# Kernel tuning notes

Hardware: AMD Instinct MI355X
Metric: run time of the kernel (lower is better)

Reference implementation:

```python
import jax, jax.numpy as jnp
import numpy as np

N_NODES = 65536
N_EDGES = 524288
N_GRAPHS = 64
PTS_PER_GRAPH = 1024


def gcn_conv(x, W, b, row, col, self_idx, n_nodes):
    # PyG GCNConv: x' = D^{-1/2} (A + I) D^{-1/2} x W + b
    xw = x @ W
    row2 = jnp.concatenate([row, self_idx])
    col2 = jnp.concatenate([col, self_idx])
    deg = jax.ops.segment_sum(jnp.ones_like(col2, dtype=xw.dtype), col2, num_segments=n_nodes)
    dinv = jax.lax.rsqrt(deg)  # deg >= 1 thanks to self-loops
    norm = dinv[row2] * dinv[col2]  # [E+N]
    out = jax.ops.segment_sum(xw[row2] * norm[:, None], col2, num_segments=n_nodes)
    return out + b


def setup_inputs() -> dict:
    key = jax.random.key(0)
    ks = jax.random.split(key, 12)

    def glorot(k, fan_in, fan_out):
        s = jnp.sqrt(6.0 / (fan_in + fan_out))
        return jax.random.uniform(k, (fan_in, fan_out), jnp.float32, -s, s)

    x = jax.random.normal(ks[0], (N_NODES, 3), jnp.float32)
    edge_index = jax.random.randint(ks[1], (2, N_EDGES), 0, N_NODES, dtype=jnp.int64)
    batch = (jnp.arange(N_NODES, dtype=jnp.int64) // PTS_PER_GRAPH)  # 64 graphs x 1024 pts

    return {
        "x": x, "edge_index": edge_index, "batch": batch,
        "W1": glorot(ks[2], 3, 64), "b1": jnp.zeros((64,), jnp.float32),
        "W2": glorot(ks[3], 64, 256), "b2": jnp.zeros((256,), jnp.float32),
        "W3": glorot(ks[4], 256, 512), "b3": jnp.zeros((512,), jnp.float32),
        "Wm1": glorot(ks[5], 1024, 512), "bm1": jnp.zeros((512,), jnp.float32),
        "Wm2": glorot(ks[6], 512, 10), "bm2": jnp.zeros((10,), jnp.float32),
    }


def reference(x, edge_index, batch, W1, b1, W2, b2, W3, b3, Wm1, bm1, Wm2, bm2):
    n = x.shape[0]
    row, col = edge_index[0], edge_index[1]
    self_idx = jnp.arange(n, dtype=edge_index.dtype)

    x1 = jax.nn.relu(gcn_conv(x, W1, b1, row, col, self_idx, n))
    x2 = jax.nn.relu(gcn_conv(x1, W2, b2, row, col, self_idx, n))
    x3 = jax.nn.relu(gcn_conv(x2, W3, b3, row, col, self_idx, n))

    # global mean / max pool over batch segments
    counts = jax.ops.segment_sum(jnp.ones((n,), x3.dtype), batch, num_segments=N_GRAPHS)
    x_mean = jax.ops.segment_sum(x3, batch, num_segments=N_GRAPHS) / counts[:, None]
    x_max = jax.ops.segment_max(x3, batch, num_segments=N_GRAPHS)
    h = jnp.concatenate([x_mean, x_max], axis=1)  # [G, 1024]

    h = jax.nn.relu(h @ Wm1 + bm1)  # dropout is identity in eval
    return h @ Wm2 + bm2  # [G, 10]
```

## Files before the change

kernel.cpp:

```cpp
#include <hip/hip_runtime.h>
#include <hip/hip_bf16.h>

typedef __hip_bfloat16 bf16;
typedef short bf16x8 __attribute__((ext_vector_type(8)));
typedef float f32x4 __attribute__((ext_vector_type(4)));

__device__ __forceinline__ float b2f_us(unsigned short u) {
    union { unsigned int i; float f; } c;
    c.i = ((unsigned int)u) << 16;
    return c.f;
}
__device__ __forceinline__ unsigned short f2b_us(float f) {
    bf16 h = __float2bfloat16(f);
    return *reinterpret_cast<unsigned short*>(&h);
}
__device__ __forceinline__ void unpack8(uint4 p, float* f) {
    f[0] = b2f_us(p.x & 0xffff); f[1] = b2f_us(p.x >> 16);
    f[2] = b2f_us(p.y & 0xffff); f[3] = b2f_us(p.y >> 16);
    f[4] = b2f_us(p.z & 0xffff); f[5] = b2f_us(p.z >> 16);
    f[6] = b2f_us(p.w & 0xffff); f[7] = b2f_us(p.w >> 16);
}

__device__ __forceinline__ void async_copy16(const bf16* g, bf16* l) {
    __builtin_amdgcn_global_load_lds(
        (const __attribute__((address_space(1))) unsigned int*)g,
        (__attribute__((address_space(3))) unsigned int*)l, 16, 0, 0);
}

__global__ __launch_bounds__(256) void k_count(const int* __restrict__ col,
                                               int* __restrict__ cnt, int E) {
    int e = blockIdx.x * 256 + threadIdx.x;
    if (e < E) atomicAdd(cnt + col[e], 1);
}
__global__ __launch_bounds__(256) void k_scan_a(const int* __restrict__ cnt,
                                                int* __restrict__ bsum,
                                                float* __restrict__ dinv) {
    __shared__ int s[256];
    int t = threadIdx.x;
    int i = blockIdx.x * 256 + t;
    int c = cnt[i];
    dinv[i] = rsqrtf((float)c + 1.0f);
    s[t] = c;
    __syncthreads();
#pragma unroll
    for (int off = 128; off >= 1; off >>= 1) {
        if (t < off) s[t] += s[t + off];
        __syncthreads();
    }
    if (t == 0) bsum[blockIdx.x] = s[0];
}
__global__ __launch_bounds__(256) void k_scan_b(const int* __restrict__ bsum,
                                                int* __restrict__ boff) {
    __shared__ int s[256];
    int t = threadIdx.x;
    int self = bsum[t];
    s[t] = self;
    __syncthreads();
#pragma unroll
    for (int off = 1; off < 256; off <<= 1) {
        int v = (t >= off) ? s[t - off] : 0;
        __syncthreads();
        s[t] += v;
        __syncthreads();
    }
    boff[t] = s[t] - self;
}
__global__ __launch_bounds__(256) void k_scan_c(const int* __restrict__ cnt,
                                                const int* __restrict__ boff,
                                                int* __restrict__ rowptr) {
    __shared__ int s[256];
    int t = threadIdx.x;
    int base = blockIdx.x * 256;
    int self = cnt[base + t];
    s[t] = self;
    __syncthreads();
#pragma unroll
    for (int off = 1; off < 256; off <<= 1) {
        int v = (t >= off) ? s[t - off] : 0;
        __syncthreads();
        s[t] += v;
        __syncthreads();
    }
    rowptr[base + t] = boff[blockIdx.x] + s[t] - self;
}

__global__ __launch_bounds__(256) void k_scatter(const int* __restrict__ row,
                                                 const int* __restrict__ col,
                                                 const float* __restrict__ dinv,
                                                 const int* __restrict__ rowptr,
                                                 int* __restrict__ fill,
                                                 int2* __restrict__ adj, int E) {
    int e = blockIdx.x * 256 + threadIdx.x;
    if (e >= E) return;
    int r = row[e], c = col[e];
    int pos = rowptr[c] + atomicAdd(fill + c, 1);
    adj[pos] = make_int2(r, __float_as_int(dinv[r]));
}

__global__ __launch_bounds__(256) void k_prep_all(const float* __restrict__ W2,
                                                  bf16* __restrict__ WT2,
                                                  const float* __restrict__ W3,
                                                  bf16* __restrict__ WT3) {
    int idx = blockIdx.x * 256 + threadIdx.x;
    if (idx < 64 * 256) {
        int k = idx >> 8, n = idx & 255;
        WT2[n * 64 + k] = __float2bfloat16(W2[idx]);
    } else {
        int i = idx - 64 * 256;
        if (i < 256 * 512) {
            int k = i >> 9, n = i & 511;
            WT3[(size_t)n * 256 + k] = __float2bfloat16(W3[i]);
        }
    }
}

__global__ __launch_bounds__(256) void k_gcn1(const int2* __restrict__ adj,
                                              const int* __restrict__ rowptr,
                                              const int* __restrict__ cnt,
                                              const float* __restrict__ dinv,
                                              const float* __restrict__ x,
                                              const float* __restrict__ W,
                                              const float* __restrict__ bias,
                                              bf16* __restrict__ h1, int N) {
    __shared__ float w[256];
    int t = threadIdx.x;
    if (t < 192) w[t] = W[t];
    else w[t] = bias[t - 192];
    __syncthreads();
    int n = blockIdx.x * 256 + t;
    if (n >= N) return;
    float d = dinv[n];
    float d2 = d * d;
    float a0 = x[n * 3] * d2, a1 = x[n * 3 + 1] * d2, a2 = x[n * 3 + 2] * d2;
    int beg = rowptr[n], end = beg + cnt[n];
    for (int e = beg; e < end; ++e) {
        int2 ad = adj[e];
        float wt = __int_as_float(ad.y) * d;
        a0 += x[ad.x * 3] * wt;
        a1 += x[ad.x * 3 + 1] * wt;
        a2 += x[ad.x * 3 + 2] * wt;
    }
    bf16* dst = h1 + (size_t)n * 64;
#pragma unroll
    for (int fb = 0; fb < 8; ++fb) {
        uint4 r;
        unsigned v[4];
#pragma unroll
        for (int p = 0; p < 4; ++p) {
            int f0 = fb * 8 + p * 2;
            float u0 = fmaxf(a0 * w[f0] + a1 * w[64 + f0] + a2 * w[128 + f0] + w[192 + f0], 0.f);
            int f1 = f0 + 1;
            float u1 = fmaxf(a0 * w[f1] + a1 * w[64 + f1] + a2 * w[128 + f1] + w[192 + f1], 0.f);
            v[p] = (unsigned)f2b_us(u0) | ((unsigned)f2b_us(u1) << 16);
        }
        r.x = v[0]; r.y = v[1]; r.z = v[2]; r.w = v[3];
        *reinterpret_cast<uint4*>(dst + fb * 8) = r;
    }
}

template <int F>
__global__ __launch_bounds__(256, 4) void k_gather_pre(const int2* __restrict__ adj,
                                                       const int* __restrict__ rowptr,
                                                       const int* __restrict__ cnt,
                                                       const float* __restrict__ dinv,
                                                       const bf16* __restrict__ h,
                                                       bf16* __restrict__ agg, int N) {
    constexpr int LPN = F / 8;
    constexpr int NPB = 256 / LPN;
    int t = threadIdx.x;
    int node = blockIdx.x * NPB + t / LPN;
    if (node >= N) return;
    int fbase = (t % LPN) * 8;
    float d = dinv[node];
    size_t sbase = (size_t)node * F + fbase;
    uint4 sp = *reinterpret_cast<const uint4*>(h + sbase);
    float a[8];
    unpack8(sp, a);
    float d2 = d * d;
#pragma unroll
    for (int i = 0; i < 8; i++) a[i] *= d2;
    int beg = rowptr[node];
    int end = beg + cnt[node];
    int e = beg;
    for (; e + 7 < end; e += 8) {
        int2 ad[8];
        uint4 p[8];
#pragma unroll
        for (int u = 0; u < 8; ++u) ad[u] = adj[e + u];
#pragma unroll
        for (int u = 0; u < 8; ++u)
            p[u] = *reinterpret_cast<const uint4*>(h + (size_t)ad[u].x * F + fbase);
#pragma unroll
        for (int u = 0; u < 8; ++u) {
            float wt = __int_as_float(ad[u].y) * d;
            float f[8];
            unpack8(p[u], f);
#pragma unroll
            for (int i = 0; i < 8; i++) a[i] += f[i] * wt;
        }
    }
    for (; e + 3 < end; e += 4) {
        int2 ad[4];
        uint4 p[4];
#pragma unroll
        for (int u = 0; u < 4; ++u) ad[u] = adj[e + u];
#pragma unroll
        for (int u = 0; u < 4; ++u)
            p[u] = *reinterpret_cast<const uint4*>(h + (size_t)ad[u].x * F + fbase);
#pragma unroll
        for (int u = 0; u < 4; ++u) {
            float wt = __int_as_float(ad[u].y) * d;
            float f[8];
            unpack8(p[u], f);
#pragma unroll
            for (int i = 0; i < 8; i++) a[i] += f[i] * wt;
        }
    }
    for (; e < end; ++e) {
        int2 ad = adj[e];
        float wt = __int_as_float(ad.y) * d;
        uint4 p = *reinterpret_cast<const uint4*>(h + (size_t)ad.x * F + fbase);
        float f[8];
        unpack8(p, f);
#pragma unroll
        for (int i = 0; i < 8; i++) a[i] += f[i] * wt;
    }
    uint4 r;
    r.x = (unsigned)f2b_us(a[0]) | ((unsigned)f2b_us(a[1]) << 16);
    r.y = (unsigned)f2b_us(a[2]) | ((unsigned)f2b_us(a[3]) << 16);
    r.z = (unsigned)f2b_us(a[4]) | ((unsigned)f2b_us(a[5]) << 16);
    r.w = (unsigned)f2b_us(a[6]) | ((unsigned)f2b_us(a[7]) << 16);
    *reinterpret_cast<uint4*>(agg + sbase) = r;
}

__global__ __launch_bounds__(256) void k_gemm_br(const bf16* __restrict__ A,
                                                 const bf16* __restrict__ BT,
                                                 const float* __restrict__ bias,
                                                 bf16* __restrict__ C,
                                                 int M, int N, int K) {
    __shared__ bf16 As[128 * 32];
    __shared__ bf16 Bs[128 * 32];
    const int t = threadIdx.x;
    const int wave = t >> 6, lane = t & 63;
    const int quad = lane >> 4, l16 = lane & 15;
    const int wm = wave & 1, wn = wave >> 1;
    const int m0 = blockIdx.x * 128;
    const int n0 = blockIdx.y * 128;

    f32x4 acc[4][4] = {};
    for (int kb = 0; kb < K; kb += 32) {
#pragma unroll
        for (int rnd = 0; rnd < 2; ++rnd) {
            int c = (rnd * 4 + wave) * 64 + lane;
            int r = c >> 2, seg = c & 3;
            async_copy16(A + (size_t)(m0 + r) * K + kb + seg * 8, As + c * 8);
            async_copy16(BT + (size_t)(n0 + r) * K + kb + seg * 8, Bs + c * 8);
        }
        __syncthreads();
        bf16x8 af[4], bfr[4];
#pragma unroll
        for (int i = 0; i < 4; i++)
            af[i] = *reinterpret_cast<const bf16x8*>(&As[(wm * 64 + i * 16 + l16) * 32 + quad * 8]);
#pragma unroll
        for (int j = 0; j < 4; j++)
            bfr[j] = *reinterpret_cast<const bf16x8*>(&Bs[(wn * 64 + j * 16 + l16) * 32 + quad * 8]);
#pragma unroll
        for (int i = 0; i < 4; i++)
#pragma unroll
            for (int j = 0; j < 4; j++)
                acc[i][j] = __builtin_amdgcn_mfma_f32_16x16x32_bf16(af[i], bfr[j], acc[i][j], 0, 0, 0);
        __syncthreads();
    }
#pragma unroll
    for (int j = 0; j < 4; j++) {
        int cn = n0 + wn * 64 + j * 16 + l16;
        float bv = bias[cn];
#pragma unroll
        for (int i = 0; i < 4; i++) {
            int row = m0 + wm * 64 + i * 16 + quad * 4;
#pragma unroll
            for (int r = 0; r < 4; r++)
                C[(size_t)(row + r) * N + cn] = __float2bfloat16(fmaxf(acc[i][j][r] + bv, 0.f));
        }
    }
}

__global__ __launch_bounds__(256) void k_gemm_pool(const bf16* __restrict__ A,
                                                   const bf16* __restrict__ BT,
                                                   const float* __restrict__ bias,
                                                   float* __restrict__ partials,
                                                   int M, int N, int K) {
    __shared__ bf16 As[128 * 32];
    __shared__ bf16 Bs[128 * 32];
    const int t = threadIdx.x;
    const int wave = t >> 6, lane = t & 63;
    const int quad = lane >> 4, l16 = lane & 15;
    const int wm = wave & 1, wn = wave >> 1;
    const int m0 = blockIdx.x * 128;
    const int n0 = blockIdx.y * 128;

    f32x4 acc[4][4] = {};
    for (int kb = 0; kb < K; kb += 32) {
#pragma unroll
        for (int rnd = 0; rnd < 2; ++rnd) {
            int c = (rnd * 4 + wave) * 64 + lane;
            int r = c >> 2, seg = c & 3;
            async_copy16(A + (size_t)(m0 + r) * K + kb + seg * 8, As + c * 8);
            async_copy16(BT + (size_t)(n0 + r) * K + kb + seg * 8, Bs + c * 8);
        }
        __syncthreads();
        bf16x8 af[4], bfr[4];
#pragma unroll
        for (int i = 0; i < 4; i++)
            af[i] = *reinterpret_cast<const bf16x8*>(&As[(wm * 64 + i * 16 + l16) * 32 + quad * 8]);
#pragma unroll
        for (int j = 0; j < 4; j++)
            bfr[j] = *reinterpret_cast<const bf16x8*>(&Bs[(wn * 64 + j * 16 + l16) * 32 + quad * 8]);
#pragma unroll
        for (int i = 0; i < 4; i++)
#pragma unroll
            for (int j = 0; j < 4; j++)
                acc[i][j] = __builtin_amdgcn_mfma_f32_16x16x32_bf16(af[i], bfr[j], acc[i][j], 0, 0, 0);
        __syncthreads();
    }
    size_t pbase = ((size_t)(blockIdx.x * 4 + blockIdx.y) * 2 + wm) * 256;
#pragma unroll
    for (int j = 0; j < 4; j++) {
        int f128 = wn * 64 + j * 16 + l16;
        float bv = bias[n0 + f128];
        float s = 0.f, mx = 0.f;
#pragma unroll
        for (int i = 0; i < 4; i++)
#pragma unroll
            for (int r = 0; r < 4; r++) {
                float v = fmaxf(acc[i][j][r] + bv, 0.f);
                s += v;
                mx = fmaxf(mx, v);
            }
        s += __shfl_xor(s, 16);
        s += __shfl_xor(s, 32);
        mx = fmaxf(mx, __shfl_xor(mx, 16));
        mx = fmaxf(mx, __shfl_xor(mx, 32));
        if (quad == 0) {
            partials[pbase + f128] = s;
            partials[pbase + 128 + f128] = mx;
        }
    }
}

__global__ __launch_bounds__(256) void k_pool_final(const float* __restrict__ partials,
                                                    float* __restrict__ pooled) {
    int idx = blockIdx.x * 256 + threadIdx.x;
    int g = idx >> 9, f = idx & 511;
    int by = f >> 7, f128 = f & 127;
    float S = 0.f, M = 0.f;
#pragma unroll
    for (int tile = 0; tile < 8; ++tile) {
        int bx = g * 8 + tile;
#pragma unroll
        for (int wm = 0; wm < 2; ++wm) {
            size_t pbase = ((size_t)(bx * 4 + by) * 2 + wm) * 256;
            S += partials[pbase + f128];
            M = fmaxf(M, partials[pbase + 128 + f128]);
        }
    }
    pooled[g * 1024 + f] = S * (1.0f / 1024.0f);
    pooled[g * 1024 + 512 + f] = M;
}

__global__ __launch_bounds__(256) void k_mlp1(const float* __restrict__ pooled,
                                              const float* __restrict__ Wm1,
                                              const float* __restrict__ bm1,
                                              float* __restrict__ o) {
    __shared__ float hg[1024];
    __shared__ float red[256];
    int g = blockIdx.x;
    int t = threadIdx.x;
    int f64 = t & 63, kq = t >> 6;
    int f = blockIdx.y * 64 + f64;
#pragma unroll
    for (int i = 0; i < 4; i++) hg[t + i * 256] = pooled[g * 1024 + t + i * 256];
    __syncthreads();
    float acc = 0.f;
    int k0 = kq * 256;
#pragma unroll 8
    for (int k = k0; k < k0 + 256; ++k)
        acc += hg[k] * Wm1[(size_t)k * 512 + f];
    red[t] = acc;
    __syncthreads();
    if (t < 64) {
        float total = red[t] + red[t + 64] + red[t + 128] + red[t + 192] + bm1[f];
        o[g * 512 + f] = fmaxf(total, 0.f);
    }
}

__global__ __launch_bounds__(512) void k_mlp2(const float* __restrict__ h,
                                              const float* __restrict__ Wm2,
                                              const float* __restrict__ bm2,
                                              float* __restrict__ out) {
    int g = blockIdx.x;
    int t = threadIdx.x;
    int j = t >> 5, lane32 = t & 31;
    float acc = 0.f;
    if (j < 10) {
        int k0 = lane32 * 16;
#pragma unroll
        for (int i = 0; i < 16; ++i)
            acc += h[g * 512 + k0 + i] * Wm2[(size_t)(k0 + i) * 10 + j];
    }
#pragma unroll
    for (int m = 16; m >= 1; m >>= 1) acc += __shfl_xor(acc, m);
    if (j < 10 && lane32 == 0) out[g * 10 + j] = acc + bm2[j];
}

extern "C" void kernel_launch(void* const* d_in, const int* in_sizes, int n_in,
                              void* d_out, int out_size, void* d_ws, size_t ws_size,
                              hipStream_t stream) {
    const float* x   = (const float*)d_in[0];
    const int*   ei  = (const int*)d_in[1];
    const float* W1  = (const float*)d_in[3];
    const float* b1  = (const float*)d_in[4];
    const float* W2  = (const float*)d_in[5];
    const float* b2  = (const float*)d_in[6];
    const float* W3  = (const float*)d_in[7];
    const float* b3  = (const float*)d_in[8];
    const float* Wm1 = (const float*)d_in[9];
    const float* bm1 = (const float*)d_in[10];
    const float* Wm2 = (const float*)d_in[11];
    const float* bm2 = (const float*)d_in[12];
    float* out = (float*)d_out;

    const int N = in_sizes[0] / 3;
    const int E = in_sizes[1] / 2;
    const int* row = ei;
    const int* col = ei + E;

    char* ws = (char*)d_ws;
    size_t off = 0;
    auto alloc = [&](size_t bytes) {
        void* p = ws + off;
        off += (bytes + 255) & ~(size_t)255;
        return p;
    };
    int*   cnt      = (int*)alloc((size_t)N * 4);
    int*   fill     = (int*)alloc((size_t)N * 4);
    int*   rowptr   = (int*)alloc((size_t)N * 4);
    float* dinv     = (float*)alloc((size_t)N * 4);
    int*   bsum     = (int*)alloc(256 * 4);
    int*   boff     = (int*)alloc(256 * 4);
    int2*  adj      = (int2*)alloc((size_t)E * 8);
    bf16*  h1       = (bf16*)alloc((size_t)N * 64 * 2);
    bf16*  agg2     = (bf16*)alloc((size_t)N * 64 * 2);
    bf16*  h2       = (bf16*)alloc((size_t)N * 256 * 2);
    bf16*  agg3     = (bf16*)alloc((size_t)N * 256 * 2);
    bf16*  WT2      = (bf16*)alloc(256 * 64 * 2);
    bf16*  WT3      = (bf16*)alloc(512 * 256 * 2);
    float* partials = (float*)alloc((size_t)512 * 4 * 2 * 256 * 4);
    float* pooled   = (float*)alloc(64 * 1024 * 4);
    float* m1       = (float*)alloc(64 * 512 * 4);

    hipMemsetAsync(cnt, 0, (size_t)N * 8, stream);
    k_count<<<(E + 255) / 256, 256, 0, stream>>>(col, cnt, E);
    k_scan_a<<<256, 256, 0, stream>>>(cnt, bsum, dinv);
    k_scan_b<<<1, 256, 0, stream>>>(bsum, boff);
    k_scan_c<<<256, 256, 0, stream>>>(cnt, boff, rowptr);
    k_scatter<<<(E + 255) / 256, 256, 0, stream>>>(row, col, dinv, rowptr, fill, adj, E);

    k_prep_all<<<(64 * 256 + 256 * 512 + 255) / 256, 256, 0, stream>>>(W2, WT2, W3, WT3);

    k_gcn1<<<(N + 255) / 256, 256, 0, stream>>>(adj, rowptr, cnt, dinv, x, W1, b1, h1, N);

    k_gather_pre<64><<<(N * 8) / 256, 256, 0, stream>>>(adj, rowptr, cnt, dinv, h1, agg2, N);
    k_gemm_br<<<dim3(N / 128, 256 / 128), 256, 0, stream>>>(agg2, WT2, b2, h2, N, 256, 64);

    k_gather_pre<256><<<(N * 32) / 256, 256, 0, stream>>>(adj, rowptr, cnt, dinv, h2, agg3, N);
    k_gemm_pool<<<dim3(N / 128, 512 / 128), 256, 0, stream>>>(agg3, WT3, b3, partials, N, 512, 256);
    k_pool_final<<<(64 * 512) / 256, 256, 0, stream>>>(partials, pooled);

    k_mlp1<<<dim3(64, 8), 256, 0, stream>>>(pooled, Wm1, bm1, m1);
    k_mlp2<<<64, 512, 0, stream>>>(m1, Wm2, bm2, out);
}
```

Before: 275.8 us.

## Split gather edge lists across two lane halves and reuse count-phase atomic ranks

```diff
diff --git a/kernel.cpp b/kernel.cpp
--- a/kernel.cpp
+++ b/kernel.cpp
@@ -4,6 +4,7 @@
 typedef __hip_bfloat16 bf16;
 typedef short bf16x8 __attribute__((ext_vector_type(8)));
 typedef float f32x4 __attribute__((ext_vector_type(4)));
+typedef unsigned int u32x4 __attribute__((ext_vector_type(4)));
 
 __device__ __forceinline__ float b2f_us(unsigned short u) {
     union { unsigned int i; float f; } c;
@@ -28,9 +29,10 @@
 }
 
 __global__ __launch_bounds__(256) void k_count(const int* __restrict__ col,
-                                               int* __restrict__ cnt, int E) {
+                                               int* __restrict__ cnt,
+                                               int* __restrict__ rank, int E) {
     int e = blockIdx.x * 256 + threadIdx.x;
-    if (e < E) atomicAdd(cnt + col[e], 1);
+    if (e < E) rank[e] = atomicAdd(cnt + col[e], 1);
 }
 __global__ __launch_bounds__(256) void k_scan_a(const int* __restrict__ cnt,
                                                 int* __restrict__ bsum,
@@ -88,12 +90,12 @@
                                                  const int* __restrict__ col,
                                                  const float* __restrict__ dinv,
                                                  const int* __restrict__ rowptr,
-                                                 int* __restrict__ fill,
+                                                 const int* __restrict__ rank,
                                                  int2* __restrict__ adj, int E) {
     int e = blockIdx.x * 256 + threadIdx.x;
     if (e >= E) return;
     int r = row[e], c = col[e];
-    int pos = rowptr[c] + atomicAdd(fill + c, 1);
+    int pos = rowptr[c] + rank[e];
     adj[pos] = make_int2(r, __float_as_int(dinv[r]));
 }
 
@@ -159,46 +161,37 @@
 }
 
 template <int F>
-__global__ __launch_bounds__(256, 4) void k_gather_pre(const int2* __restrict__ adj,
+__global__ __launch_bounds__(256, 8) void k_gather_pre(const int2* __restrict__ adj,
                                                        const int* __restrict__ rowptr,
                                                        const int* __restrict__ cnt,
                                                        const float* __restrict__ dinv,
                                                        const bf16* __restrict__ h,
                                                        bf16* __restrict__ agg, int N) {
     constexpr int LPN = F / 8;
-    constexpr int NPB = 256 / LPN;
-    int t = threadIdx.x;
-    int node = blockIdx.x * NPB + t / LPN;
+    constexpr int GRP = 2 * LPN;
+    constexpr int NPB = 256 / GRP;
+    int t = threadIdx.x;
+    int node = blockIdx.x * NPB + t / GRP;
     if (node >= N) return;
-    int fbase = (t % LPN) * 8;
+    int gl = t % GRP;
+    int fs = gl % LPN;
+    int half = gl / LPN;
+    int fbase = fs * 8;
     float d = dinv[node];
     size_t sbase = (size_t)node * F + fbase;
-    uint4 sp = *reinterpret_cast<const uint4*>(h + sbase);
-    float a[8];
-    unpack8(sp, a);
-    float d2 = d * d;
-#pragma unroll
-    for (int i = 0; i < 8; i++) a[i] *= d2;
+    float a[8] = {0.f, 0.f, 0.f, 0.f, 0.f, 0.f, 0.f, 0.f};
+    if (half == 0) {
+        uint4 sp = *reinterpret_cast<const uint4*>(h + sbase);
+        unpack8(sp, a);
+        float d2 = d * d;
+#pragma unroll
+        for (int i = 0; i < 8; i++) a[i] *= d2;
+    }
     int beg = rowptr[node];
-    int end = beg + cnt[node];
-    int e = beg;
-    for (; e + 7 < end; e += 8) {
-        int2 ad[8];
-        uint4 p[8];
-#pragma unroll
-        for (int u = 0; u < 8; ++u) ad[u] = adj[e + u];
-#pragma unroll
-        for (int u = 0; u < 8; ++u)
-            p[u] = *reinterpret_cast<const uint4*>(h + (size_t)ad[u].x * F + fbase);
-#pragma unroll
-        for (int u = 0; u < 8; ++u) {
-            float wt = __int_as_float(ad[u].y) * d;
-            float f[8];
-            unpack8(p[u], f);
-#pragma unroll
-            for (int i = 0; i < 8; i++) a[i] += f[i] * wt;
-        }
-    }
+    int deg = cnt[node];
+    int mid = beg + ((deg + 1) >> 1);
+    int e   = half ? mid : beg;
+    int end = half ? (beg + deg) : mid;
     for (; e + 3 < end; e += 4) {
         int2 ad[4];
         uint4 p[4];
@@ -225,12 +218,16 @@
 #pragma unroll
         for (int i = 0; i < 8; i++) a[i] += f[i] * wt;
     }
-    uint4 r;
-    r.x = (unsigned)f2b_us(a[0]) | ((unsigned)f2b_us(a[1]) << 16);
-    r.y = (unsigned)f2b_us(a[2]) | ((unsigned)f2b_us(a[3]) << 16);
-    r.z = (unsigned)f2b_us(a[4]) | ((unsigned)f2b_us(a[5]) << 16);
-    r.w = (unsigned)f2b_us(a[6]) | ((unsigned)f2b_us(a[7]) << 16);
-    *reinterpret_cast<uint4*>(agg + sbase) = r;
+#pragma unroll
+    for (int i = 0; i < 8; i++) a[i] += __shfl_xor(a[i], LPN);
+    if (half == 0) {
+        u32x4 r;
+        r.x = (unsigned)f2b_us(a[0]) | ((unsigned)f2b_us(a[1]) << 16);
+        r.y = (unsigned)f2b_us(a[2]) | ((unsigned)f2b_us(a[3]) << 16);
+        r.z = (unsigned)f2b_us(a[4]) | ((unsigned)f2b_us(a[5]) << 16);
+        r.w = (unsigned)f2b_us(a[6]) | ((unsigned)f2b_us(a[7]) << 16);
+        __builtin_nontemporal_store(r, reinterpret_cast<u32x4*>(agg + sbase));
+    }
 }
 
 __global__ __launch_bounds__(256) void k_gemm_br(const bf16* __restrict__ A,
@@ -443,11 +440,11 @@
         return p;
     };
     int*   cnt      = (int*)alloc((size_t)N * 4);
-    int*   fill     = (int*)alloc((size_t)N * 4);
     int*   rowptr   = (int*)alloc((size_t)N * 4);
     float* dinv     = (float*)alloc((size_t)N * 4);
     int*   bsum     = (int*)alloc(256 * 4);
     int*   boff     = (int*)alloc(256 * 4);
+    int*   rank     = (int*)alloc((size_t)E * 4);
     int2*  adj      = (int2*)alloc((size_t)E * 8);
     bf16*  h1       = (bf16*)alloc((size_t)N * 64 * 2);
     bf16*  agg2     = (bf16*)alloc((size_t)N * 64 * 2);
@@ -459,21 +456,21 @@
     float* pooled   = (float*)alloc(64 * 1024 * 4);
     float* m1       = (float*)alloc(64 * 512 * 4);
 
-    hipMemsetAsync(cnt, 0, (size_t)N * 8, stream);
-    k_count<<<(E + 255) / 256, 256, 0, stream>>>(col, cnt, E);
+    (void)hipMemsetAsync(cnt, 0, (size_t)N * 4, stream);
+    k_count<<<(E + 255) / 256, 256, 0, stream>>>(col, cnt, rank, E);
     k_scan_a<<<256, 256, 0, stream>>>(cnt, bsum, dinv);
     k_scan_b<<<1, 256, 0, stream>>>(bsum, boff);
     k_scan_c<<<256, 256, 0, stream>>>(cnt, boff, rowptr);
-    k_scatter<<<(E + 255) / 256, 256, 0, stream>>>(row, col, dinv, rowptr, fill, adj, E);
+    k_scatter<<<(E + 255) / 256, 256, 0, stream>>>(row, col, dinv, rowptr, rank, adj, E);
 
     k_prep_all<<<(64 * 256 + 256 * 512 + 255) / 256, 256, 0, stream>>>(W2, WT2, W3, WT3);
 
     k_gcn1<<<(N + 255) / 256, 256, 0, stream>>>(adj, rowptr, cnt, dinv, x, W1, b1, h1, N);
 
-    k_gather_pre<64><<<(N * 8) / 256, 256, 0, stream>>>(adj, rowptr, cnt, dinv, h1, agg2, N);
+    k_gather_pre<64><<<(N * 16) / 256, 256, 0, stream>>>(adj, rowptr, cnt, dinv, h1, agg2, N);
     k_gemm_br<<<dim3(N / 128, 256 / 128), 256, 0, stream>>>(agg2, WT2, b2, h2, N, 256, 64);
 
-    k_gather_pre<256><<<(N * 32) / 256, 256, 0, stream>>>(adj, rowptr, cnt, dinv, h2, agg3, N);
+    k_gather_pre<256><<<(N * 64) / 256, 256, 0, stream>>>(adj, rowptr, cnt, dinv, h2, agg3, N);
     k_gemm_pool<<<dim3(N / 128, 512 / 128), 256, 0, stream>>>(agg3, WT3, b3, partials, N, 512, 256);
     k_pool_final<<<(64 * 512) / 256, 256, 0, stream>>>(partials, pooled);
 
```

Measured after the change: 259.9 us. -5.8%, faster.
